# Kernel optimization log

Measured on AMD Instinct MI355X. Metric: run time of the kernel, lower is better.

## Reference

```python
import jax, jax.numpy as jnp
import numpy as np

N_NODES = 100000
N_EDGES = 3200000
# (out_dim, in_dim) for the 4 BayesianLinear layers: mlp1 = [5->16, 16->32], mlp2 = [35->16, 16->1]
LAYER_DIMS = [(16, 5), (32, 16), (16, 35), (1, 16)]


def setup_inputs() -> dict:
    key = jax.random.key(0)
    ks = iter(jax.random.split(key, 32))
    inp = {}
    inp["x"] = jax.random.normal(next(ks), (N_NODES, 3), jnp.float32)
    inp["edge_attr"] = jax.random.normal(next(ks), (N_EDGES, 2), jnp.float32)
    inp["edge_index"] = jax.random.randint(next(ks), (2, N_EDGES), 0, N_NODES, dtype=jnp.int64)
    for li, (o, i) in enumerate(LAYER_DIMS, 1):
        inp[f"l{li}_wmu"] = jax.random.normal(next(ks), (o, i), jnp.float32) * 0.1
        inp[f"l{li}_wrho"] = jax.random.normal(next(ks), (o, i), jnp.float32) * 0.1 - 5.0
        inp[f"l{li}_bmu"] = jax.random.normal(next(ks), (o,), jnp.float32) * 0.1
        inp[f"l{li}_brho"] = jax.random.normal(next(ks), (o,), jnp.float32) * 0.1 - 5.0
        inp[f"l{li}_eps_w"] = jax.random.normal(next(ks), (o, i), jnp.float32)
        inp[f"l{li}_eps_b"] = jax.random.normal(next(ks), (o,), jnp.float32)
    return inp


def _bayes_linear(h, wmu, wrho, bmu, brho, eps_w, eps_b):
    # sampled weight: W = mu + softplus(rho) * eps  (blitz BayesianLinear)
    W = wmu + jax.nn.softplus(wrho) * eps_w          # [out, in]
    b = bmu + jax.nn.softplus(brho) * eps_b          # [out]
    return h @ W.T + b


def _igconv(x, edge_index, edge_attr, p1, p2, p3, p4):
    src, dst = edge_index[0], edge_index[1]          # x_j = x[src], aggregate at dst
    x_j = x[src]                                     # [E, 3] irregular gather
    m = jnp.concatenate([x_j, edge_attr], axis=1)    # [E, 5]
    m = jax.nn.relu(_bayes_linear(m, *p1))           # [E, 16]
    m = jax.nn.relu(_bayes_linear(m, *p2))           # [E, 32]
    agg = jax.ops.segment_max(m, dst, num_segments=x.shape[0])  # [N, 32]
    agg = jnp.where(jnp.isneginf(agg), 0.0, agg)     # nodes with no in-edges -> 0
    h = jnp.concatenate([x, agg], axis=1)            # [N, 35]
    h = jax.nn.relu(_bayes_linear(h, *p3))           # [N, 16]
    comb = jax.nn.sigmoid(_bayes_linear(h, *p4))     # [N, 1]
    return jnp.concatenate([x[:, :2], comb], axis=1) # [N, 3]


def reference(x, edge_attr, edge_index,
              l1_wmu, l1_wrho, l1_bmu, l1_brho, l1_eps_w, l1_eps_b,
              l2_wmu, l2_wrho, l2_bmu, l2_brho, l2_eps_w, l2_eps_b,
              l3_wmu, l3_wrho, l3_bmu, l3_brho, l3_eps_w, l3_eps_b,
              l4_wmu, l4_wrho, l4_bmu, l4_brho, l4_eps_w, l4_eps_b):
    p1 = (l1_wmu, l1_wrho, l1_bmu, l1_brho, l1_eps_w, l1_eps_b)
    p2 = (l2_wmu, l2_wrho, l2_bmu, l2_brho, l2_eps_w, l2_eps_b)
    p3 = (l3_wmu, l3_wrho, l3_bmu, l3_brho, l3_eps_w, l3_eps_b)
    p4 = (l4_wmu, l4_wrho, l4_bmu, l4_brho, l4_eps_w, l4_eps_b)
    h = x
    for _ in range(3):  # three stacked applications of the same IGConv
        h = _igconv(h, edge_index, edge_attr, p1, p2, p3, p4)
    return h
```

## Files before the change

kernel.cpp:

```cpp
#include <hip/hip_runtime.h>
#include <math.h>

#define WTOT  1233
#define PKOFS 1280
#define PKTOT 352

typedef __fp16 h2 __attribute__((ext_vector_type(2)));
typedef __fp16 f16x8 __attribute__((ext_vector_type(8)));
typedef float f32x16 __attribute__((ext_vector_type(16)));

struct ERec { int s; int d; unsigned int ea; };

__device__ __forceinline__ h2 u2h(unsigned int u) { return __builtin_bit_cast(h2, u); }
__device__ __forceinline__ unsigned int h2u(h2 h) { return __builtin_bit_cast(unsigned int, h); }
#define DOT2(a, b, c) __builtin_amdgcn_fdot2((a), (b), (c), false)

__device__ __forceinline__ float softplus_f(float x) {
  return fmaxf(x, 0.f) + log1pf(expf(-fabsf(x)));
}

struct PrepArgs {
  const float* wmu[4]; const float* wrho[4]; const float* epsw[4];
  const float* bmu[4]; const float* brho[4]; const float* epsb[4];
  float* out; int* bucketCur; int nbuck;
};

__global__ void prep_all_kernel(PrepArgs a) {
  const int wsz[4] = {80, 512, 560, 16};
  const int wof[4] = {0, 96, 640, 1216};
  const int bsz[4] = {16, 32, 16, 1};
  const int bof[4] = {80, 608, 1200, 1232};
  float* wg = a.out;
  int tid = threadIdx.x;
  if (tid < a.nbuck) a.bucketCur[tid] = 0;
#pragma unroll
  for (int l = 0; l < 4; l++) {
    for (int i = tid; i < wsz[l]; i += 1024)
      wg[wof[l] + i] = a.wmu[l][i] + softplus_f(a.wrho[l][i]) * a.epsw[l][i];
    for (int i = tid; i < bsz[l]; i += 1024)
      wg[bof[l] + i] = a.bmu[l][i] + softplus_f(a.brho[l][i]) * a.epsb[l][i];
  }
  __syncthreads();
  unsigned int* wp = (unsigned int*)(wg + PKOFS);
  int t = tid;
  if (t < 16) {
    wp[t]      = h2u(h2{(__fp16)wg[t * 5 + 0], (__fp16)wg[t * 5 + 1]});
    wp[16 + t] = h2u(h2{(__fp16)wg[t * 5 + 2], (__fp16)0.f});
    wp[32 + t] = h2u(h2{(__fp16)wg[t * 5 + 3], (__fp16)wg[t * 5 + 4]});
    ((float*)wp)[304 + t] = wg[80 + t];
  }
  if (t < 32) {
    ((float*)wp)[320 + t] = wg[608 + t];
    for (int j = 0; j < 8; j++)
      wp[48 + t * 8 + j] =
          h2u(h2{(__fp16)wg[96 + t * 16 + 2 * j], (__fp16)wg[96 + t * 16 + 2 * j + 1]});
  }
}

__global__ __launch_bounds__(1024) void bhist_kernel(const int* __restrict__ dst,
                                                     int* __restrict__ bucketCur,
                                                     int E, int NBUCK) {
  __shared__ int h[1024];
  int tid = threadIdx.x;
  for (int i = tid; i < NBUCK; i += 1024) h[i] = 0;
  __syncthreads();
  int base = blockIdx.x * 8192;
#pragma unroll
  for (int r = 0; r < 8; r++) {
    int e = base + r * 1024 + tid;
    if (e < E) atomicAdd(&h[dst[e] >> 8], 1);
  }
  __syncthreads();
  for (int i = tid; i < NBUCK; i += 1024) {
    int c = h[i];
    if (c) atomicAdd(&bucketCur[i], c);
  }
}

__global__ __launch_bounds__(1024) void scanBk_kernel(int* __restrict__ bucketCur,
                                                      int* __restrict__ bucketOff,
                                                      int NBUCK) {
  __shared__ int wsum[16];
  __shared__ int woff[16];
  int tid = threadIdx.x, lane = tid & 63, wid = tid >> 6;
  int v = (tid < NBUCK) ? bucketCur[tid] : 0;
  int x = v;
#pragma unroll
  for (int off = 1; off < 64; off <<= 1) {
    int t = __shfl_up(x, off, 64);
    if (lane >= off) x += t;
  }
  if (lane == 63) wsum[wid] = x;
  __syncthreads();
  if (wid == 0) {
    int s = (lane < 16) ? wsum[lane] : 0;
#pragma unroll
    for (int off = 1; off < 16; off <<= 1) {
      int t = __shfl_up(s, off, 64);
      if (lane >= off) s += t;
    }
    if (lane < 16) woff[lane] = s - wsum[lane];
  }
  __syncthreads();
  int excl = woff[wid] + x - v;
  if (tid < NBUCK) {
    bucketOff[tid] = excl;
    bucketCur[tid] = excl;
    if (tid == NBUCK - 1) bucketOff[NBUCK] = excl + v;
  }
}

__global__ __launch_bounds__(1024) void part_kernel(
    const int* __restrict__ src, const int* __restrict__ dst,
    const float2* __restrict__ ea, int* __restrict__ bucketCur,
    ERec* __restrict__ brec, int E, int NBUCK) {
  __shared__ int h[1024];
  int tid = threadIdx.x;
  for (int i = tid; i < NBUCK; i += 1024) h[i] = 0;
  __syncthreads();
  int base = blockIdx.x * 8192;
  int d[8], s[8];
  unsigned int a[8];
  bool v[8];
#pragma unroll
  for (int j = 0; j < 8; j++) {
    int e = base + j * 1024 + tid;
    v[j] = e < E;
    if (v[j]) {
      d[j] = dst[e];
      s[j] = src[e];
      float2 t = ea[e];
      a[j] = h2u(__builtin_amdgcn_cvt_pkrtz(t.x, t.y));
      atomicAdd(&h[d[j] >> 8], 1);
    }
  }
  __syncthreads();
  for (int i = tid; i < NBUCK; i += 1024) {
    int c = h[i];
    h[i] = c ? atomicAdd(&bucketCur[i], c) : 0;
  }
  __syncthreads();
#pragma unroll
  for (int j = 0; j < 8; j++) {
    if (v[j]) {
      int pos = atomicAdd(&h[d[j] >> 8], 1);
      ERec t; t.s = s[j]; t.d = d[j]; t.ea = a[j];
      brec[pos] = t;
    }
  }
}

__global__ __launch_bounds__(512) void deg_kernel(const ERec* __restrict__ brec,
                                                  const int* __restrict__ bucketOff,
                                                  int* __restrict__ deg, int N) {
  __shared__ int cnt[256];
  int b = blockIdx.x, tid = threadIdx.x;
  if (tid < 256) cnt[tid] = 0;
  __syncthreads();
  int e0 = bucketOff[b], e1 = bucketOff[b + 1];
  for (int i = e0 + tid; i < e1; i += 512) atomicAdd(&cnt[brec[i].d & 255], 1);
  __syncthreads();
  int node = b * 256 + tid;
  if (tid < 256 && node < N) deg[node] = cnt[tid];
}

__global__ void scanA_kernel(const int* __restrict__ deg, int* __restrict__ part, int n) {
  __shared__ int ws[16];
  int tid = threadIdx.x;
  int i = blockIdx.x * 1024 + tid;
  int v = 0;
  if (i < n) v = (deg[i] + 3) & ~3;
#pragma unroll
  for (int off = 32; off >= 1; off >>= 1) v += __shfl_down(v, off, 64);
  if ((tid & 63) == 0) ws[tid >> 6] = v;
  __syncthreads();
  if (tid == 0) {
    int s = 0;
#pragma unroll
    for (int k = 0; k < 16; k++) s += ws[k];
    part[blockIdx.x] = s;
  }
}

__global__ void scanB_kernel(int* __restrict__ part, int P, int* __restrict__ etot) {
  int lane = threadIdx.x;
  int carry = 0;
  for (int base = 0; base < P; base += 64) {
    int i = base + lane;
    int v = (i < P) ? part[i] : 0;
    int x = v;
#pragma unroll
    for (int off = 1; off < 64; off <<= 1) {
      int t = __shfl_up(x, off, 64);
      if (lane >= off) x += t;
    }
    if (i < P) part[i] = carry + x - v;
    carry += __shfl(x, 63, 64);
  }
  if (lane == 0) *etot = carry;
}

__global__ void scanC_kernel(const int* __restrict__ deg, const int* __restrict__ part,
                             int* __restrict__ cursor, int n) {
  __shared__ int wsum[16];
  __shared__ int woff[16];
  int tid = threadIdx.x, lane = tid & 63, wid = tid >> 6;
  int i = blockIdx.x * 1024 + tid;
  int v = 0;
  if (i < n) v = (deg[i] + 3) & ~3;
  int x = v;
#pragma unroll
  for (int off = 1; off < 64; off <<= 1) {
    int t = __shfl_up(x, off, 64);
    if (lane >= off) x += t;
  }
  if (lane == 63) wsum[wid] = x;
  __syncthreads();
  if (wid == 0) {
    int s = (lane < 16) ? wsum[lane] : 0;
#pragma unroll
    for (int off = 1; off < 16; off <<= 1) {
      int t = __shfl_up(s, off, 64);
      if (lane >= off) s += t;
    }
    if (lane < 16) woff[lane] = s - wsum[lane];
  }
  __syncthreads();
  if (i < n) cursor[i] = part[blockIdx.x] + woff[wid] + x - v;
}

__global__ __launch_bounds__(512) void scat_kernel(
    const ERec* __restrict__ brec, const int* __restrict__ bucketOff,
    const int* __restrict__ cursor, ERec* __restrict__ erec, int N) {
  __shared__ int lcur[256];
  int b = blockIdx.x, tid = threadIdx.x;
  int node = b * 256 + tid;
  if (tid < 256) lcur[tid] = (node < N) ? cursor[node] : 0;
  __syncthreads();
  int e0 = bucketOff[b], e1 = bucketOff[b + 1];
  for (int i = e0 + tid; i < e1; i += 512) {
    ERec t = brec[i];
    int pos = atomicAdd(&lcur[t.d & 255], 1);
    erec[pos] = t;
  }
  __syncthreads();
  if (tid < 256 && node < N) {
    int cur = cursor[node];
    int endR = lcur[tid];
    int endP = cur + ((endR - cur + 3) & ~3);
    if (endR > cur) {
      ERec rep = erec[cur];
      for (int k = endR; k < endP; k++) erec[k] = rep;
    }
  }
}

__global__ void xpack_kernel(const float* __restrict__ x, uint2* __restrict__ xpk,
                             unsigned int* __restrict__ agg32, int n) {
  int i = blockIdx.x * blockDim.x + threadIdx.x;
  if (i < n) {
    h2 a = __builtin_amdgcn_cvt_pkrtz(x[3 * i], x[3 * i + 1]);
    h2 b = __builtin_amdgcn_cvt_pkrtz(x[3 * i + 2], 0.f);
    xpk[i] = make_uint2(h2u(a), h2u(b));
    uint4 z = make_uint4(0u, 0u, 0u, 0u);
    uint4* ap = (uint4*)(agg32 + (size_t)i * 32);
#pragma unroll
    for (int k = 0; k < 8; k++) ap[k] = z;
    if (i == 0) {
      uint4* as = (uint4*)(agg32 + (size_t)n * 32);
#pragma unroll
      for (int k = 0; k < 8; k++) as[k] = z;
    }
  }
}

__global__ __launch_bounds__(256) void edge_kernel(
    const uint2* __restrict__ xpk, const ERec* __restrict__ erec,
    unsigned int* __restrict__ agg32,
    const float* __restrict__ wg, const int* __restrict__ pEtot, int N) {
  __shared__ __align__(16) unsigned int lds[4][64][12];
  const unsigned int* wp = (const unsigned int*)(wg + PKOFS);
  const float* bf = (const float*)wp;
  const int Etot = *pEtot;
  if (blockIdx.x * 256 >= Etot) return;
  const int tid = threadIdx.x;
  const int lane = tid & 63;
  const int wslot = tid >> 6;
  const int e = blockIdx.x * 256 + tid;

  bool vld = e < Etot;
  ERec r;
  r.s = 0; r.d = N; r.ea = 0u;
  if (vld) r = erec[e];
  int d = r.d;
  uint2 xs = xpk[r.s];

  h2 p01 = u2h(xs.x), p2v = u2h(xs.y), pea = u2h(r.ea);
  unsigned int m1[8];
#pragma unroll
  for (int p = 0; p < 8; p++) {
    const int oA = 2 * p, oB = 2 * p + 1;
    float sA = DOT2(p01, u2h(wp[oA]),
                DOT2(p2v, u2h(wp[16 + oA]),
                DOT2(pea, u2h(wp[32 + oA]), bf[304 + oA])));
    float sB = DOT2(p01, u2h(wp[oB]),
                DOT2(p2v, u2h(wp[16 + oB]),
                DOT2(pea, u2h(wp[32 + oB]), bf[304 + oB])));
    m1[p] = h2u(__builtin_amdgcn_cvt_pkrtz(fmaxf(sA, 0.f), fmaxf(sB, 0.f)));
  }

  uint4* rowp = (uint4*)&lds[wslot][lane][0];
  rowp[0] = make_uint4(m1[0], m1[1], m1[2], m1[3]);
  rowp[1] = make_uint4(m1[4], m1[5], m1[6], m1[7]);
  asm volatile("s_waitcnt lgkmcnt(0)" ::: "memory");
  __builtin_amdgcn_sched_barrier(0);

  const int col = lane & 31;
  const int h = lane >> 5;
  f16x8 bfrag = __builtin_bit_cast(f16x8, *(const uint4*)&wp[48 + col * 8 + 4 * h]);
  float bias = bf[320 + col];
  f32x16 cini;
#pragma unroll
  for (int i = 0; i < 16; i++) cini[i] = bias;

  f16x8 a0 = __builtin_bit_cast(f16x8, *(const uint4*)&lds[wslot][col][4 * h]);
  f16x8 a1 = __builtin_bit_cast(f16x8, *(const uint4*)&lds[wslot][32 + col][4 * h]);
  f32x16 acc0 = __builtin_amdgcn_mfma_f32_32x32x16_f16(a0, bfrag, cini, 0, 0, 0);
  f32x16 acc1 = __builtin_amdgcn_mfma_f32_32x32x16_f16(a1, bfrag, cini, 0, 0, 0);

  float bm[2][4];
#pragma unroll
  for (int q = 0; q < 4; q++) {
    bm[0][q] = fmaxf(fmaxf(acc0[4 * q], acc0[4 * q + 1]),
                     fmaxf(acc0[4 * q + 2], fmaxf(acc0[4 * q + 3], 0.f)));
    bm[1][q] = fmaxf(fmaxf(acc1[4 * q], acc1[4 * q + 1]),
                     fmaxf(acc1[4 * q + 2], fmaxf(acc1[4 * q + 3], 0.f)));
  }

  int dp4 = __shfl_up(d, 4, 64);
  bool isHead = ((lane & 3) == 0) && (lane == 0 || d != dp4);
  unsigned long long hm = __ballot(isHead);

  unsigned long long rem = hm;
  while (rem) {
    int a = (int)__builtin_ctzll(rem);
    rem &= rem - 1;
    int b = rem ? (int)__builtin_ctzll(rem) : 64;
    int rd = __shfl(d, a, 64);
    int A = a >> 2, B = b >> 2;
    float mx = 0.f;
#pragma unroll
    for (int g = 0; g < 2; g++) {
#pragma unroll
      for (int q = 0; q < 4; q++) {
        int blk = 8 * g + 2 * q + h;
        bool in = (blk >= A) && (blk < B);
        mx = fmaxf(mx, in ? bm[g][q] : 0.f);
      }
    }
    mx = fmaxf(mx, __shfl_xor(mx, 32, 64));
    if (lane < 32 && rd < N)
      atomicMax(agg32 + (size_t)rd * 32 + col, __float_as_uint(mx));
  }
}

__global__ __launch_bounds__(256) void node_kernel(
    const float* __restrict__ x, const float* __restrict__ cin,
    float* __restrict__ cout, uint2* __restrict__ xpk,
    float* __restrict__ outFinal, unsigned int* __restrict__ agg32,
    const float* __restrict__ wg, int n) {
  int nid = blockIdx.x * blockDim.x + threadIdx.x;
  if (nid >= n) return;
  uint4* ap = (uint4*)(agg32 + (size_t)nid * 32);
  uint4 q[8];
#pragma unroll
  for (int i = 0; i < 8; i++) q[i] = ap[i];
  uint4 z = make_uint4(0u, 0u, 0u, 0u);
#pragma unroll
  for (int i = 0; i < 8; i++) ap[i] = z;
  float av[32];
#pragma unroll
  for (int i = 0; i < 8; i++) {
    av[4 * i + 0] = __uint_as_float(q[i].x);
    av[4 * i + 1] = __uint_as_float(q[i].y);
    av[4 * i + 2] = __uint_as_float(q[i].z);
    av[4 * i + 3] = __uint_as_float(q[i].w);
  }
  float x0 = x[3 * nid], x1 = x[3 * nid + 1];
  float x2 = cin ? cin[nid] : x[3 * nid + 2];
  float h[16];
#pragma unroll
  for (int o = 0; o < 16; o++) {
    float sa = wg[1200 + o];
    sa = fmaf(wg[640 + o * 35 + 0], x0, sa);
    sa = fmaf(wg[640 + o * 35 + 1], x1, sa);
    sa = fmaf(wg[640 + o * 35 + 2], x2, sa);
#pragma unroll
    for (int k = 0; k < 32; k++) sa = fmaf(wg[640 + o * 35 + 3 + k], av[k], sa);
    h[o] = fmaxf(sa, 0.f);
  }
  float z4 = wg[1232];
#pragma unroll
  for (int k = 0; k < 16; k++) z4 = fmaf(wg[1216 + k], h[k], z4);
  float comb = 1.f / (1.f + expf(-z4));
  cout[nid] = comb;
  ((unsigned int*)xpk)[2 * nid + 1] = h2u(__builtin_amdgcn_cvt_pkrtz(comb, 0.f));
  if (outFinal) {
    outFinal[3 * nid] = x0;
    outFinal[3 * nid + 1] = x1;
    outFinal[3 * nid + 2] = comb;
  }
}

extern "C" void kernel_launch(void* const* d_in, const int* in_sizes, int n_in,
                              void* d_out, int out_size, void* d_ws, size_t ws_size,
                              hipStream_t stream) {
  const float* x = (const float*)d_in[0];
  const float* ea = (const float*)d_in[1];
  const int* eidx = (const int*)d_in[2];
  const int N = in_sizes[0] / 3;
  const int E = in_sizes[1] / 2;
  const int* src = eidx;
  const int* dst = eidx + E;
  const int P = (N + 1023) / 1024;
  const int NBUCK = (N + 255) >> 8;
  const int EP = E + 3 * N;

  char* p = (char*)d_ws;
  size_t off = 0;
  auto alloc = [&](size_t bytes) -> char* {
    char* r = p + off;
    off = (off + bytes + 255) & ~(size_t)255;
    return r;
  };
  float* wbuf = (float*)alloc((size_t)(PKOFS + PKTOT) * 4);
  int* deg = (int*)alloc((size_t)N * 4);
  int* part = (int*)alloc((size_t)P * 4);
  int* cursor = (int*)alloc((size_t)N * 4);
  int* bucketOff = (int*)alloc(((size_t)NBUCK + 1) * 4);
  int* bucketCur = (int*)alloc((size_t)NBUCK * 4);
  int* etot = (int*)alloc(4);
  ERec* erec = (ERec*)alloc((size_t)EP * sizeof(ERec));
  char* uni = alloc((size_t)E * 12);
  ERec* brec = (ERec*)uni;
  size_t uoff = 0;
  auto ualloc = [&](size_t bytes) -> char* {
    char* r = uni + uoff;
    uoff = (uoff + bytes + 255) & ~(size_t)255;
    return r;
  };
  unsigned int* agg32 = (unsigned int*)ualloc(((size_t)N + 1) * 32 * 4);
  uint2* xpk = (uint2*)ualloc((size_t)N * 8);
  float* bufA = (float*)ualloc((size_t)N * 4);
  float* bufB = (float*)ualloc((size_t)N * 4);
  (void)ws_size;

  PrepArgs pa;
  for (int l = 0; l < 4; l++) {
    pa.wmu[l] = (const float*)d_in[3 + 6 * l + 0];
    pa.wrho[l] = (const float*)d_in[3 + 6 * l + 1];
    pa.bmu[l] = (const float*)d_in[3 + 6 * l + 2];
    pa.brho[l] = (const float*)d_in[3 + 6 * l + 3];
    pa.epsw[l] = (const float*)d_in[3 + 6 * l + 4];
    pa.epsb[l] = (const float*)d_in[3 + 6 * l + 5];
  }
  pa.out = wbuf;
  pa.bucketCur = bucketCur;
  pa.nbuck = NBUCK;

  const int TB = 256;
  auto blocks = [&](int n) { return dim3((n + TB - 1) / TB); };

  prep_all_kernel<<<dim3(1), dim3(1024), 0, stream>>>(pa);
  bhist_kernel<<<dim3((E + 8191) / 8192), dim3(1024), 0, stream>>>(dst, bucketCur, E, NBUCK);
  scanBk_kernel<<<dim3(1), dim3(1024), 0, stream>>>(bucketCur, bucketOff, NBUCK);
  part_kernel<<<dim3((E + 8191) / 8192), dim3(1024), 0, stream>>>(
      src, dst, (const float2*)ea, bucketCur, brec, E, NBUCK);
  deg_kernel<<<dim3(NBUCK), dim3(512), 0, stream>>>(brec, bucketOff, deg, N);
  scanA_kernel<<<dim3(P), dim3(1024), 0, stream>>>(deg, part, N);
  scanB_kernel<<<dim3(1), dim3(64), 0, stream>>>(part, P, etot);
  scanC_kernel<<<dim3(P), dim3(1024), 0, stream>>>(deg, part, cursor, N);
  scat_kernel<<<dim3(NBUCK), dim3(512), 0, stream>>>(brec, bucketOff, cursor, erec, N);
  xpack_kernel<<<blocks(N), dim3(TB), 0, stream>>>(x, xpk, agg32, N);

  float* outp = (float*)d_out;
  const int ebp = (EP + 255) / 256;
  edge_kernel<<<dim3(ebp), dim3(TB), 0, stream>>>(xpk, erec, agg32, wbuf, etot, N);
  node_kernel<<<blocks(N), dim3(TB), 0, stream>>>(x, nullptr, bufA, xpk, nullptr,
                                                  agg32, wbuf, N);
  edge_kernel<<<dim3(ebp), dim3(TB), 0, stream>>>(xpk, erec, agg32, wbuf, etot, N);
  node_kernel<<<blocks(N), dim3(TB), 0, stream>>>(x, bufA, bufB, xpk, nullptr,
                                                  agg32, wbuf, N);
  edge_kernel<<<dim3(ebp), dim3(TB), 0, stream>>>(xpk, erec, agg32, wbuf, etot, N);
  node_kernel<<<blocks(N), dim3(TB), 0, stream>>>(x, bufB, bufA, xpk, outp,
                                                  agg32, wbuf, N);
}
```

Before: 364.6 us.

## Fuse degree/scan/scatter into one kernel and tag aggregation slots per layer

Degree counting, the three-stage exclusive scan and the scatter kernels are merged into a single per-bucket kernel. It computes local degrees in LDS and obtains its global base from an atomicAdd on a running edge total, which removes four launches and the deg/part/cursor buffers. The aggregation buffer now stores a 2-bit layer tag in the high bits of each max value, so node_kernel no longer zeroes agg32 after reading it. In exchange, per-node edge ranges are no longer in node order, and values lose one mantissa bit from the shift.

```diff
diff --git a/kernel.cpp b/kernel.cpp
--- a/kernel.cpp
+++ b/kernel.cpp
@@ -22,7 +22,7 @@
 struct PrepArgs {
   const float* wmu[4]; const float* wrho[4]; const float* epsw[4];
   const float* bmu[4]; const float* brho[4]; const float* epsb[4];
-  float* out; int* bucketCur; int nbuck;
+  float* out; int* bucketCur; int* etot; int nbuck;
 };
 
 __global__ void prep_all_kernel(PrepArgs a) {
@@ -33,6 +33,7 @@
   float* wg = a.out;
   int tid = threadIdx.x;
   if (tid < a.nbuck) a.bucketCur[tid] = 0;
+  if (tid == 1023) *a.etot = 0;
 #pragma unroll
   for (int l = 0; l < 4; l++) {
     for (int i = tid; i < wsz[l]; i += 1024)
@@ -150,106 +151,60 @@
   }
 }
 
-__global__ __launch_bounds__(512) void deg_kernel(const ERec* __restrict__ brec,
-                                                  const int* __restrict__ bucketOff,
-                                                  int* __restrict__ deg, int N) {
+__global__ __launch_bounds__(1024) void scat_kernel(
+    const ERec* __restrict__ brec, const int* __restrict__ bucketOff,
+    int* __restrict__ etot, ERec* __restrict__ erec, int N) {
   __shared__ int cnt[256];
+  __shared__ int sstart[256];
+  __shared__ int wsum[4];
+  __shared__ int woff[4];
+  __shared__ int sbase;
   int b = blockIdx.x, tid = threadIdx.x;
+  int lane = tid & 63, wid = tid >> 6;
   if (tid < 256) cnt[tid] = 0;
   __syncthreads();
   int e0 = bucketOff[b], e1 = bucketOff[b + 1];
-  for (int i = e0 + tid; i < e1; i += 512) atomicAdd(&cnt[brec[i].d & 255], 1);
-  __syncthreads();
-  int node = b * 256 + tid;
-  if (tid < 256 && node < N) deg[node] = cnt[tid];
-}
-
-__global__ void scanA_kernel(const int* __restrict__ deg, int* __restrict__ part, int n) {
-  __shared__ int ws[16];
-  int tid = threadIdx.x;
-  int i = blockIdx.x * 1024 + tid;
+  for (int i = e0 + tid; i < e1; i += 1024) atomicAdd(&cnt[brec[i].d & 255], 1);
+  __syncthreads();
   int v = 0;
-  if (i < n) v = (deg[i] + 3) & ~3;
-#pragma unroll
-  for (int off = 32; off >= 1; off >>= 1) v += __shfl_down(v, off, 64);
-  if ((tid & 63) == 0) ws[tid >> 6] = v;
-  __syncthreads();
-  if (tid == 0) {
-    int s = 0;
-#pragma unroll
-    for (int k = 0; k < 16; k++) s += ws[k];
-    part[blockIdx.x] = s;
-  }
-}
-
-__global__ void scanB_kernel(int* __restrict__ part, int P, int* __restrict__ etot) {
-  int lane = threadIdx.x;
-  int carry = 0;
-  for (int base = 0; base < P; base += 64) {
-    int i = base + lane;
-    int v = (i < P) ? part[i] : 0;
-    int x = v;
-#pragma unroll
-    for (int off = 1; off < 64; off <<= 1) {
-      int t = __shfl_up(x, off, 64);
-      if (lane >= off) x += t;
-    }
-    if (i < P) part[i] = carry + x - v;
-    carry += __shfl(x, 63, 64);
-  }
-  if (lane == 0) *etot = carry;
-}
-
-__global__ void scanC_kernel(const int* __restrict__ deg, const int* __restrict__ part,
-                             int* __restrict__ cursor, int n) {
-  __shared__ int wsum[16];
-  __shared__ int woff[16];
-  int tid = threadIdx.x, lane = tid & 63, wid = tid >> 6;
-  int i = blockIdx.x * 1024 + tid;
-  int v = 0;
-  if (i < n) v = (deg[i] + 3) & ~3;
+  if (tid < 256) v = (cnt[tid] + 3) & ~3;
   int x = v;
 #pragma unroll
   for (int off = 1; off < 64; off <<= 1) {
     int t = __shfl_up(x, off, 64);
     if (lane >= off) x += t;
   }
-  if (lane == 63) wsum[wid] = x;
-  __syncthreads();
-  if (wid == 0) {
-    int s = (lane < 16) ? wsum[lane] : 0;
-#pragma unroll
-    for (int off = 1; off < 16; off <<= 1) {
+  if (tid < 256 && lane == 63) wsum[wid] = x;
+  __syncthreads();
+  if (wid == 0 && lane < 4) {
+    int s = wsum[lane];
+#pragma unroll
+    for (int off = 1; off < 4; off <<= 1) {
       int t = __shfl_up(s, off, 64);
       if (lane >= off) s += t;
     }
-    if (lane < 16) woff[lane] = s - wsum[lane];
-  }
-  __syncthreads();
-  if (i < n) cursor[i] = part[blockIdx.x] + woff[wid] + x - v;
-}
-
-__global__ __launch_bounds__(512) void scat_kernel(
-    const ERec* __restrict__ brec, const int* __restrict__ bucketOff,
-    const int* __restrict__ cursor, ERec* __restrict__ erec, int N) {
-  __shared__ int lcur[256];
-  int b = blockIdx.x, tid = threadIdx.x;
-  int node = b * 256 + tid;
-  if (tid < 256) lcur[tid] = (node < N) ? cursor[node] : 0;
-  __syncthreads();
-  int e0 = bucketOff[b], e1 = bucketOff[b + 1];
-  for (int i = e0 + tid; i < e1; i += 512) {
+    woff[lane] = s - wsum[lane];
+    if (lane == 3) sbase = atomicAdd(etot, s);
+  }
+  __syncthreads();
+  if (tid < 256) {
+    int start = sbase + woff[wid] + x - v;
+    sstart[tid] = start;
+    cnt[tid] = start;
+  }
+  __syncthreads();
+  for (int i = e0 + tid; i < e1; i += 1024) {
     ERec t = brec[i];
-    int pos = atomicAdd(&lcur[t.d & 255], 1);
+    int pos = atomicAdd(&cnt[t.d & 255], 1);
     erec[pos] = t;
   }
   __syncthreads();
-  if (tid < 256 && node < N) {
-    int cur = cursor[node];
-    int endR = lcur[tid];
-    int endP = cur + ((endR - cur + 3) & ~3);
-    if (endR > cur) {
-      ERec rep = erec[cur];
+  if (tid < 256) {
+    int start = sstart[tid];
+    int endR = cnt[tid];
+    int endP = start + ((endR - start + 3) & ~3);
+    if (endR > start) {
+      ERec rep = erec[start];
       for (int k = endR; k < endP; k++) erec[k] = rep;
     }
   }
@@ -277,7 +232,8 @@
 __global__ __launch_bounds__(256) void edge_kernel(
     const uint2* __restrict__ xpk, const ERec* __restrict__ erec,
     unsigned int* __restrict__ agg32,
-    const float* __restrict__ wg, const int* __restrict__ pEtot, int N) {
+    const float* __restrict__ wg, const int* __restrict__ pEtot,
+    unsigned int tag, int N) {
   __shared__ __align__(16) unsigned int lds[4][64][12];
   const unsigned int* wp = (const unsigned int*)(wg + PKOFS);
   const float* bf = (const float*)wp;
@@ -359,32 +315,33 @@
       }
     }
     mx = fmaxf(mx, __shfl_xor(mx, 32, 64));
-    if (lane < 32 && rd < N)
-      atomicMax(agg32 + (size_t)rd * 32 + col, __float_as_uint(mx));
+    if (lane < 32 && rd < N) {
+      unsigned int bits = __float_as_uint(mx);
+      atomicMax(agg32 + (size_t)rd * 32 + col, (tag << 30) | (bits >> 1));
+    }
   }
 }
 
 __global__ __launch_bounds__(256) void node_kernel(
     const float* __restrict__ x, const float* __restrict__ cin,
     float* __restrict__ cout, uint2* __restrict__ xpk,
-    float* __restrict__ outFinal, unsigned int* __restrict__ agg32,
-    const float* __restrict__ wg, int n) {
+    float* __restrict__ outFinal, const unsigned int* __restrict__ agg32,
+    const float* __restrict__ wg, unsigned int tag, int n) {
   int nid = blockIdx.x * blockDim.x + threadIdx.x;
   if (nid >= n) return;
-  uint4* ap = (uint4*)(agg32 + (size_t)nid * 32);
+  const uint4* ap = (const uint4*)(agg32 + (size_t)nid * 32);
   uint4 q[8];
 #pragma unroll
   for (int i = 0; i < 8; i++) q[i] = ap[i];
-  uint4 z = make_uint4(0u, 0u, 0u, 0u);
-#pragma unroll
-  for (int i = 0; i < 8; i++) ap[i] = z;
   float av[32];
 #pragma unroll
   for (int i = 0; i < 8; i++) {
-    av[4 * i + 0] = __uint_as_float(q[i].x);
-    av[4 * i + 1] = __uint_as_float(q[i].y);
-    av[4 * i + 2] = __uint_as_float(q[i].z);
-    av[4 * i + 3] = __uint_as_float(q[i].w);
+    unsigned int w[4] = {q[i].x, q[i].y, q[i].z, q[i].w};
+#pragma unroll
+    for (int j = 0; j < 4; j++) {
+      unsigned int u = ((w[j] >> 30) == tag) ? ((w[j] & 0x3FFFFFFFu) << 1) : 0u;
+      av[4 * i + j] = __uint_as_float(u);
+    }
   }
   float x0 = x[3 * nid], x1 = x[3 * nid + 1];
   float x2 = cin ? cin[nid] : x[3 * nid + 2];
@@ -422,7 +379,6 @@
   const int E = in_sizes[1] / 2;
   const int* src = eidx;
   const int* dst = eidx + E;
-  const int P = (N + 1023) / 1024;
   const int NBUCK = (N + 255) >> 8;
   const int EP = E + 3 * N;
 
@@ -434,9 +390,6 @@
     return r;
   };
   float* wbuf = (float*)alloc((size_t)(PKOFS + PKTOT) * 4);
-  int* deg = (int*)alloc((size_t)N * 4);
-  int* part = (int*)alloc((size_t)P * 4);
-  int* cursor = (int*)alloc((size_t)N * 4);
   int* bucketOff = (int*)alloc(((size_t)NBUCK + 1) * 4);
   int* bucketCur = (int*)alloc((size_t)NBUCK * 4);
   int* etot = (int*)alloc(4);
@@ -466,6 +419,7 @@
   }
   pa.out = wbuf;
   pa.bucketCur = bucketCur;
+  pa.etot = etot;
   pa.nbuck = NBUCK;
 
   const int TB = 256;
@@ -476,22 +430,18 @@
   scanBk_kernel<<<dim3(1), dim3(1024), 0, stream>>>(bucketCur, bucketOff, NBUCK);
   part_kernel<<<dim3((E + 8191) / 8192), dim3(1024), 0, stream>>>(
       src, dst, (const float2*)ea, bucketCur, brec, E, NBUCK);
-  deg_kernel<<<dim3(NBUCK), dim3(512), 0, stream>>>(brec, bucketOff, deg, N);
-  scanA_kernel<<<dim3(P), dim3(1024), 0, stream>>>(deg, part, N);
-  scanB_kernel<<<dim3(1), dim3(64), 0, stream>>>(part, P, etot);
-  scanC_kernel<<<dim3(P), dim3(1024), 0, stream>>>(deg, part, cursor, N);
-  scat_kernel<<<dim3(NBUCK), dim3(512), 0, stream>>>(brec, bucketOff, cursor, erec, N);
+  scat_kernel<<<dim3(NBUCK), dim3(1024), 0, stream>>>(brec, bucketOff, etot, erec, N);
   xpack_kernel<<<blocks(N), dim3(TB), 0, stream>>>(x, xpk, agg32, N);
 
   float* outp = (float*)d_out;
   const int ebp = (EP + 255) / 256;
-  edge_kernel<<<dim3(ebp), dim3(TB), 0, stream>>>(xpk, erec, agg32, wbuf, etot, N);
+  edge_kernel<<<dim3(ebp), dim3(TB), 0, stream>>>(xpk, erec, agg32, wbuf, etot, 1u, N);
   node_kernel<<<blocks(N), dim3(TB), 0, stream>>>(x, nullptr, bufA, xpk, nullptr,
-                                                  agg32, wbuf, N);
-  edge_kernel<<<dim3(ebp), dim3(TB), 0, stream>>>(xpk, erec, agg32, wbuf, etot, N);
+                                                  agg32, wbuf, 1u, N);
+  edge_kernel<<<dim3(ebp), dim3(TB), 0, stream>>>(xpk, erec, agg32, wbuf, etot, 2u, N);
   node_kernel<<<blocks(N), dim3(TB), 0, stream>>>(x, bufA, bufB, xpk, nullptr,
-                                                  agg32, wbuf, N);
-  edge_kernel<<<dim3(ebp), dim3(TB), 0, stream>>>(xpk, erec, agg32, wbuf, etot, N);
+                                                  agg32, wbuf, 2u, N);
+  edge_kernel<<<dim3(ebp), dim3(TB), 0, stream>>>(xpk, erec, agg32, wbuf, etot, 3u, N);
   node_kernel<<<blocks(N), dim3(TB), 0, stream>>>(x, bufB, bufA, xpk, outp,
-                                                  agg32, wbuf, N);
-}
+                                                  agg32, wbuf, 3u, N);
+}
```

Result: faster. 352.4 us (-3.4%).
